# Kernel optimization log

Measured on AMD Instinct MI355X. Metric: run time of the kernel, lower is better.

The kernel has to match this reference:

```python
import jax, jax.numpy as jnp
import numpy as np

B = 16384
OBS = 568        # 36 self features + 19 * 28 other-agent features
H = 256          # hidden_dim
SELF_DIM = 36
OTHER_DIM = 28
N_OTHER = (OBS - SELF_DIM) // OTHER_DIM  # 19


def _linear_init(key, fan_in, fan_out):
    # torch nn.Linear default: U(-1/sqrt(fan_in), 1/sqrt(fan_in))
    kw, kb = jax.random.split(key)
    s = 1.0 / np.sqrt(fan_in)
    W = jax.random.uniform(kw, (fan_in, fan_out), jnp.float32, -s, s)
    b = jax.random.uniform(kb, (fan_out,), jnp.float32, -s, s)
    return W, b


def setup_inputs() -> dict:
    key = jax.random.key(0)
    ks = jax.random.split(key, 10)
    x = jax.random.normal(ks[0], (B, OBS), jnp.float32)
    eps = jax.random.normal(ks[1], (B, H), jnp.float32)
    W_mu, b_mu = _linear_init(ks[2], OBS, H)
    W_var, b_var = _linear_init(ks[3], OBS, H)
    W_self, b_self = _linear_init(ks[4], SELF_DIM, H)
    W_other, b_other = _linear_init(ks[5], OTHER_DIM, H)
    W_q, b_q = _linear_init(ks[6], H, H)
    W_k, b_k = _linear_init(ks[7], H, H)
    W_v, b_v = _linear_init(ks[8], 2 * H, H)
    W_a, b_a = _linear_init(ks[9], 2 * H, H)
    return {"x": x, "eps": eps,
            "W_mu": W_mu, "b_mu": b_mu, "W_var": W_var, "b_var": b_var,
            "W_self": W_self, "b_self": b_self, "W_other": W_other, "b_other": b_other,
            "W_q": W_q, "b_q": b_q, "W_k": W_k, "b_k": b_k,
            "W_v": W_v, "b_v": b_v, "W_a": W_a, "b_a": b_a}


def reference(x, eps, W_mu, b_mu, W_var, b_var, W_self, b_self,
              W_other, b_other, W_q, b_q, W_k, b_k, W_v, b_v, W_a, b_a):
    relu = jax.nn.relu
    # VAE reparameterization (detach=False path)
    mu = x @ W_mu + b_mu                                  # [B, H]
    log_var = x @ W_var + b_var                           # [B, H]
    z = eps * jnp.exp(0.5 * log_var) + mu                 # [B, H]

    self_info = x[:, :SELF_DIM]                           # [B, 36]
    agents_info = x[:, SELF_DIM:].reshape(B, N_OTHER, OTHER_DIM)  # [B, N, 28]

    self_em = relu(self_info @ W_self + b_self)           # [B, H]
    other_ems = relu(agents_info @ W_other + b_other)     # [B, N, H]

    q = relu(z @ W_q + b_q)                               # [B, H]
    k = relu(other_ems @ W_k + b_k)                       # [B, N, H]
    v_in = jnp.concatenate(
        [other_ems, jnp.broadcast_to(self_em[:, None, :], (B, N_OTHER, H))], axis=-1)
    v = relu(v_in @ W_v + b_v)                            # [B, N, H]

    scores = jnp.einsum('bh,bnh->bn', q, k) / np.sqrt(H)  # [B, N]
    att_weight = jax.nn.softmax(scores, axis=-1)          # [B, N]
    h = jnp.einsum('bn,bnh->bh', att_weight, v)           # [B, H]

    out = relu(jnp.concatenate([h, self_em], axis=-1) @ W_a + b_a)  # [B, H]
    return out, att_weight[:, None, :]                    # att: [B, 1, N]
```

## Files before the change

### kernel.cpp

```cpp
#include <hip/hip_runtime.h>

typedef __bf16 bf16;
typedef __bf16 bf16x4 __attribute__((ext_vector_type(4)));
typedef __bf16 bf16x8 __attribute__((ext_vector_type(8)));
typedef float  f32x4  __attribute__((ext_vector_type(4)));

#define NB    16384
#define NOBS  568
#define NH    256
#define NAG   19

#define OFF_WT_MU    0u
#define OFF_WT_VAR   294912u
#define OFF_WT_SELF  589824u
#define OFF_WT_OTHER 622592u
#define OFF_WT_Q     638976u
#define OFF_WT_K     770048u
#define OFF_WT_V1    901120u
#define OFF_WT_V2    1032192u
#define OFF_WT_A1    1163264u
#define OFF_WT_A2    1294336u
#define OFF_Z        1425408u
#define OFF_SELF     9814016u
#define OFF_Q        18202624u
#define OFF_SV       26591232u
#define OFF_H        34979840u

static __device__ __forceinline__ unsigned short bfbits(float v) {
  bf16 b = (bf16)v;
  union { bf16 b; unsigned short u; } cvt; cvt.b = b; return cvt.u;
}

static __device__ __forceinline__ void gload16(const bf16* g, bf16* l) {
  __builtin_amdgcn_global_load_lds(
      (const __attribute__((address_space(1))) void*)g,
      (__attribute__((address_space(3))) void*)(void*)l, 16, 0, 0);
}

__global__ __launch_bounds__(256) void wprep(
    const float* __restrict__ Wmu, const float* __restrict__ Wvar,
    const float* __restrict__ Wself, const float* __restrict__ Wother,
    const float* __restrict__ Wq, const float* __restrict__ Wk,
    const float* __restrict__ Wv, const float* __restrict__ Wa, char* wsb)
{
  const float* src; bf16* dst; int K, Kp; bool chunked = false;
  switch (blockIdx.y) {
    case 0: src = Wmu;        dst = (bf16*)(wsb + OFF_WT_MU);    K = 568; Kp = 576; break;
    case 1: src = Wvar;       dst = (bf16*)(wsb + OFF_WT_VAR);   K = 568; Kp = 576; break;
    case 2: src = Wself;      dst = (bf16*)(wsb + OFF_WT_SELF);  K = 36;  Kp = 64;  break;
    case 3: src = Wother;     dst = (bf16*)(wsb + OFF_WT_OTHER); K = 28;  Kp = 32;  break;
    case 4: src = Wq;         dst = (bf16*)(wsb + OFF_WT_Q);     K = 256; Kp = 256; chunked = true; break;
    case 5: src = Wk;         dst = (bf16*)(wsb + OFF_WT_K);     K = 256; Kp = 256; chunked = true; break;
    case 6: src = Wv;         dst = (bf16*)(wsb + OFF_WT_V1);    K = 256; Kp = 256; chunked = true; break;
    case 7: src = Wv + 65536; dst = (bf16*)(wsb + OFF_WT_V2);    K = 256; Kp = 256; chunked = true; break;
    case 8: src = Wa;         dst = (bf16*)(wsb + OFF_WT_A1);    K = 256; Kp = 256; chunked = true; break;
    default: src = Wa + 65536; dst = (bf16*)(wsb + OFF_WT_A2);   K = 256; Kp = 256; chunked = true; break;
  }
  int total = 256 * Kp;
  if (chunked) {
    for (int i = blockIdx.x * 256 + threadIdx.x; i < total; i += gridDim.x * 256) {
      int ch = i >> 13, n = (i >> 5) & 255, kk = i & 31;
      int k = ch * 32 + kk;
      dst[i] = (bf16)src[k * 256 + n];
    }
  } else {
    for (int i = blockIdx.x * 256 + threadIdx.x; i < total; i += gridDim.x * 256) {
      int n = i / Kp, k = i - n * Kp;
      dst[i] = (k < K) ? (bf16)src[k * 256 + n] : (bf16)0.f;
    }
  }
}

__global__ __launch_bounds__(256, 3) void gemm_zself(
    const float* __restrict__ x,
    const bf16* __restrict__ WtMu, const bf16* __restrict__ WtVar,
    const bf16* __restrict__ WtSelf,
    const float* __restrict__ b_mu, const float* __restrict__ b_var,
    const float* __restrict__ b_self, const float* __restrict__ eps,
    bf16* __restrict__ zout, bf16* __restrict__ selfout)
{
  __shared__ bf16 ldsA[64 * 40];
  __shared__ bf16 ldsB[128 * 40];
  __shared__ bf16 ldsB2[128 * 40];

  const int tid = threadIdx.x;
  const int wave = tid >> 6;
  const int lane = tid & 63;
  const int quad = lane >> 4;
  const int m = lane & 15;
  const int rowbase = blockIdx.x * 64;
  const int colbase = (blockIdx.y & 1) * 128;
  const bool isZ = blockIdx.y < 2;
  const int K = isZ ? 576 : 64;
  const bf16* __restrict__ Wt = isZ ? WtMu : WtSelf;
  const float* __restrict__ bias = isZ ? b_mu : b_self;

  f32x4 acc[8], accB[8];
  const f32x4 z4 = {0.f, 0.f, 0.f, 0.f};
#pragma unroll
  for (int ct = 0; ct < 8; ++ct) { acc[ct] = z4; accB[ct] = z4; }

  for (int kc = 0; kc < K; kc += 32) {
    __syncthreads();
    {
#pragma unroll
      for (int it = 0; it < 2; ++it) {
        int p = tid + 256 * it;
        int r = p >> 3, fs = p & 7;
        int k = kc + fs * 4;
        const float* src = x + (size_t)(rowbase + r) * 568 + k;
        float v0, v1, v2, v3;
        if (k + 4 <= 568) {
          float4 v = *(const float4*)src;
          v0 = v.x; v1 = v.y; v2 = v.z; v3 = v.w;
        } else {
          v0 = (k + 0 < 568) ? src[0] : 0.f;
          v1 = (k + 1 < 568) ? src[1] : 0.f;
          v2 = (k + 2 < 568) ? src[2] : 0.f;
          v3 = (k + 3 < 568) ? src[3] : 0.f;
        }
        bf16x4 o = {(bf16)v0, (bf16)v1, (bf16)v2, (bf16)v3};
        *(bf16x4*)(ldsA + r * 40 + fs * 4) = o;
      }
    }
#pragma unroll
    for (int it = 0; it < 2; ++it) {
      int p = tid + 256 * it;
      int n = p >> 2, f = p & 3;
      *(bf16x8*)(ldsB + n * 40 + f * 8) =
          *(const bf16x8*)(Wt + (size_t)(colbase + n) * K + kc + f * 8);
    }
    if (isZ) {
#pragma unroll
      for (int it = 0; it < 2; ++it) {
        int p = tid + 256 * it;
        int n = p >> 2, f = p & 3;
        *(bf16x8*)(ldsB2 + n * 40 + f * 8) =
            *(const bf16x8*)(WtVar + (size_t)(colbase + n) * 576 + kc + f * 8);
      }
    }
    __syncthreads();
    bf16x8 afrag = *(const bf16x8*)(ldsA + (wave * 16 + m) * 40 + quad * 8);
#pragma unroll
    for (int ct = 0; ct < 8; ++ct) {
      bf16x8 bfrag = *(const bf16x8*)(ldsB + (ct * 16 + m) * 40 + quad * 8);
      acc[ct] = __builtin_amdgcn_mfma_f32_16x16x32_bf16(afrag, bfrag, acc[ct], 0, 0, 0);
      if (isZ) {
        bf16x8 b2 = *(const bf16x8*)(ldsB2 + (ct * 16 + m) * 40 + quad * 8);
        accB[ct] = __builtin_amdgcn_mfma_f32_16x16x32_bf16(afrag, b2, accB[ct], 0, 0, 0);
      }
    }
  }
#pragma unroll
  for (int ct = 0; ct < 8; ++ct) {
    const int col = colbase + ct * 16 + m;
    const float bv = bias[col];
#pragma unroll
    for (int r = 0; r < 4; ++r) {
      const size_t row = (size_t)rowbase + wave * 16 + quad * 4 + r;
      float v = acc[ct][r] + bv;
      if (isZ) {
        float lv = accB[ct][r] + b_var[col];
        float zz = eps[row * 256 + col] * __expf(0.5f * lv) + v;
        zout[row * 256 + col] = (bf16)zz;
      } else {
        selfout[row * 256 + col] = (bf16)(v > 0.f ? v : 0.f);
      }
    }
  }
}

__global__ __launch_bounds__(256, 4) void gemm_qsv(
    const bf16* __restrict__ zb, const bf16* __restrict__ selfb,
    const bf16* __restrict__ WtQc, const bf16* __restrict__ WtV2c,
    const float* __restrict__ b_q, const float* __restrict__ b_v,
    bf16* __restrict__ qout, bf16* __restrict__ svout)
{
  __shared__ __align__(16) bf16 lA[2][64 * 32];
  __shared__ __align__(16) bf16 lB[2][128 * 32];

  const int tid = threadIdx.x;
  const int wave = tid >> 6;
  const int lane = tid & 63;
  const int quad = lane >> 4;
  const int m = lane & 15;
  const int rowbase = blockIdx.x * 64;
  const int colbase = (blockIdx.y & 1) * 128;
  const bool isQ = blockIdx.y < 2;
  const bf16* __restrict__ Ap = isQ ? zb : selfb;
  const bf16* __restrict__ Wc = isQ ? WtQc : WtV2c;
  const float* __restrict__ bias = isQ ? b_q : b_v;
  bf16* __restrict__ outp = isQ ? qout : svout;

  f32x4 acc[8];
  const f32x4 z4 = {0.f, 0.f, 0.f, 0.f};
#pragma unroll
  for (int ct = 0; ct < 8; ++ct) acc[ct] = z4;

  const size_t arow = (size_t)(rowbase + (tid >> 2)) * 256 + (tid & 3) * 8;
  const size_t bbase = (size_t)colbase * 32 + (size_t)tid * 8;

  gload16(Ap + arow, &lA[0][wave * 512]);
  gload16(Wc + bbase, &lB[0][wave * 512]);
  gload16(Wc + bbase + 2048, &lB[0][2048 + wave * 512]);
  __syncthreads();

#pragma unroll
  for (int ch = 0; ch < 8; ++ch) {
    const int cur = ch & 1;
    if (ch < 7) {
      const int nxt = cur ^ 1;
      const size_t cof = (size_t)(ch + 1) * 8192;
      gload16(Ap + arow + (ch + 1) * 32, &lA[nxt][wave * 512]);
      gload16(Wc + cof + bbase, &lB[nxt][wave * 512]);
      gload16(Wc + cof + bbase + 2048, &lB[nxt][2048 + wave * 512]);
    }
    bf16x8 afrag = *(const bf16x8*)(&lA[cur][(wave * 16 + m) * 32 + quad * 8]);
#pragma unroll
    for (int ct = 0; ct < 8; ++ct) {
      bf16x8 bfrag = *(const bf16x8*)(&lB[cur][(ct * 16 + m) * 32 + quad * 8]);
      acc[ct] = __builtin_amdgcn_mfma_f32_16x16x32_bf16(afrag, bfrag, acc[ct], 0, 0, 0);
    }
    __syncthreads();
  }

#pragma unroll
  for (int ct = 0; ct < 8; ++ct) {
    const int col = colbase + ct * 16 + m;
    const float bv = bias[col];
#pragma unroll
    for (int r = 0; r < 4; ++r) {
      const size_t row = (size_t)rowbase + wave * 16 + quad * 4 + r;
      float v = acc[ct][r] + bv;
      if (isQ) v = (v > 0.f ? v : 0.f);
      outp[row * 256 + col] = (bf16)v;
    }
  }
}

__global__ __launch_bounds__(256, 4) void gemm_dualA(
    const bf16* __restrict__ A1, const bf16* __restrict__ A2,
    const bf16* __restrict__ Wt1c, const bf16* __restrict__ Wt2c,
    const float* __restrict__ bias, float* __restrict__ outp)
{
  __shared__ __align__(16) bf16 lA[2][64 * 32];
  __shared__ __align__(16) bf16 lB[2][128 * 32];

  const int tid = threadIdx.x;
  const int wave = tid >> 6;
  const int lane = tid & 63;
  const int quad = lane >> 4;
  const int m = lane & 15;
  const int rowbase = blockIdx.x * 64;
  const int colbase = blockIdx.y * 128;

  f32x4 acc[8];
  const f32x4 z4 = {0.f, 0.f, 0.f, 0.f};
#pragma unroll
  for (int ct = 0; ct < 8; ++ct) acc[ct] = z4;

  const size_t arow = (size_t)(rowbase + (tid >> 2)) * 256 + (tid & 3) * 8;
  const size_t bbase = (size_t)colbase * 32 + (size_t)tid * 8;

  auto stageT = [&](int buf, int t) {
    const int ch = t & 7;
    const bf16* Astep = (t < 8) ? A1 : A2;
    const bf16* Wstep = (t < 8) ? Wt1c : Wt2c;
    const size_t cof = (size_t)ch * 8192;
    gload16(Astep + arow + ch * 32, &lA[buf][wave * 512]);
    gload16(Wstep + cof + bbase, &lB[buf][wave * 512]);
    gload16(Wstep + cof + bbase + 2048, &lB[buf][2048 + wave * 512]);
  };

  stageT(0, 0);
  __syncthreads();

#pragma unroll
  for (int t = 0; t < 16; ++t) {
    const int cur = t & 1;
    if (t < 15) stageT(cur ^ 1, t + 1);
    bf16x8 afrag = *(const bf16x8*)(&lA[cur][(wave * 16 + m) * 32 + quad * 8]);
#pragma unroll
    for (int ct = 0; ct < 8; ++ct) {
      bf16x8 bfrag = *(const bf16x8*)(&lB[cur][(ct * 16 + m) * 32 + quad * 8]);
      acc[ct] = __builtin_amdgcn_mfma_f32_16x16x32_bf16(afrag, bfrag, acc[ct], 0, 0, 0);
    }
    __syncthreads();
  }

#pragma unroll
  for (int ct = 0; ct < 8; ++ct) {
    const int col = colbase + ct * 16 + m;
    const float bv = bias[col];
#pragma unroll
    for (int r = 0; r < 4; ++r) {
      const size_t row = (size_t)rowbase + wave * 16 + quad * 4 + r;
      float v = acc[ct][r] + bv;
      outp[row * 256 + col] = (v > 0.f ? v : 0.f);
    }
  }
}

__global__ __launch_bounds__(512, 4) void k_fused(
    const float* __restrict__ x, const bf16* __restrict__ qb,
    const bf16* __restrict__ svb,
    const bf16* __restrict__ WtOther, const float* __restrict__ b_other,
    const bf16* __restrict__ WtKc, const float* __restrict__ b_k,
    const bf16* __restrict__ WtVc,
    float* __restrict__ att_out, bf16* __restrict__ hb)
{
  __shared__ bf16 ldsO[80 * 264];
  __shared__ bf16 ldsA1[80 * 40];
  __shared__ bf16 qh16[1024];
  __shared__ bf16 svl16[1024];
  float* spart = (float*)ldsA1;
  float* attl  = (float*)ldsA1 + 320;

  const int tid = threadIdx.x, wave = tid >> 6, lane = tid & 63;
  const int quad = lane >> 4, m = lane & 15;
  const int b0 = blockIdx.x * 4;
  const int kvw = wave & 3;
  const bool isV = wave >= 4;

  ((unsigned*)qh16)[tid]  = ((const unsigned*)(qb  + (size_t)b0 * 256))[tid];
  ((unsigned*)svl16)[tid] = ((const unsigned*)(svb + (size_t)b0 * 256))[tid];
  for (int i = tid; i < 80 * 16; i += 512) {
    int r = i >> 4, kk = (i & 15) * 2;
    int n = r >> 2, bb = r & 3;
    float v0 = 0.f, v1 = 0.f;
    if (n < 19) {
      const float* base = x + (size_t)(b0 + bb) * NOBS + 36 + n * 28;
      if (kk < 28) v0 = base[kk];
      if (kk + 1 < 28) v1 = base[kk + 1];
    }
    unsigned u0 = bfbits(v0), u1 = bfbits(v1);
    *(unsigned*)(ldsA1 + r * 40 + kk) = u0 | (u1 << 16);
  }

  const f32x4 z4 = {0.f, 0.f, 0.f, 0.f};

  const bf16* __restrict__ Bc = isV ? WtVc : WtKc;
  const int cb = (kvw * 64 + m) * 32 + quad * 8;
  bf16x8 bE[4];
#pragma unroll
  for (int c = 0; c < 4; ++c) bE[c] = *(const bf16x8*)(Bc + cb + c * 512);

  __syncthreads();

  {
    float bo[2];
    bf16x8 bfr[2];
#pragma unroll
    for (int c = 0; c < 2; ++c) {
      int col = (2 * wave + c) * 16 + m;
      bo[c] = b_other[col];
      bfr[c] = *(const bf16x8*)(WtOther + col * 32 + quad * 8);
    }
    f32x4 acc1[5][2];
#pragma unroll
    for (int rt = 0; rt < 5; ++rt) {
      bf16x8 a = *(const bf16x8*)(ldsA1 + (rt * 16 + m) * 40 + quad * 8);
#pragma unroll
      for (int c = 0; c < 2; ++c)
        acc1[rt][c] = __builtin_amdgcn_mfma_f32_16x16x32_bf16(a, bfr[c], z4, 0, 0, 0);
    }
#pragma unroll
    for (int rt = 0; rt < 5; ++rt)
#pragma unroll
      for (int c = 0; c < 2; ++c) {
        int col = (2 * wave + c) * 16 + m;
#pragma unroll
        for (int r = 0; r < 4; ++r) {
          float v = acc1[rt][c][r] + bo[c];
          v = v > 0.f ? v : 0.f;
          unsigned u = bfbits(v);
          unsigned other = (unsigned)__shfl_xor((int)u, 1, 64);
          if ((m & 1) == 0) {
            int rowl = rt * 16 + quad * 4 + r;
            *(unsigned*)(ldsO + rowl * 264 + col) = u | (other << 16);
          }
        }
      }
  }
  __syncthreads();

  f32x4 acc[5][4];
#pragma unroll
  for (int rt = 0; rt < 5; ++rt)
#pragma unroll
    for (int c = 0; c < 4; ++c) acc[rt][c] = z4;

  {
#pragma unroll 1
    for (int ch = 0; ch < 8; ch += 2) {
      bf16x8 bO[4];
#pragma unroll
      for (int c = 0; c < 4; ++c)
        bO[c] = *(const bf16x8*)(Bc + (size_t)(ch + 1) * 8192 + cb + c * 512);
      const int kc0 = ch * 32;
#pragma unroll
      for (int rt = 0; rt < 5; ++rt) {
        bf16x8 a = *(const bf16x8*)(ldsO + (rt * 16 + m) * 264 + kc0 + quad * 8);
#pragma unroll
        for (int c = 0; c < 4; ++c)
          acc[rt][c] = __builtin_amdgcn_mfma_f32_16x16x32_bf16(a, bE[c], acc[rt][c], 0, 0, 0);
      }
#pragma unroll
      for (int c = 0; c < 4; ++c)
        bE[c] = *(const bf16x8*)(Bc + (size_t)(ch + 2) * 8192 + cb + c * 512);
      const int kc1 = kc0 + 32;
#pragma unroll
      for (int rt = 0; rt < 5; ++rt) {
        bf16x8 a = *(const bf16x8*)(ldsO + (rt * 16 + m) * 264 + kc1 + quad * 8);
#pragma unroll
        for (int c = 0; c < 4; ++c)
          acc[rt][c] = __builtin_amdgcn_mfma_f32_16x16x32_bf16(a, bO[c], acc[rt][c], 0, 0, 0);
      }
    }
  }

  if (!isV) {
    float qreg[4][4], bkreg[4];
#pragma unroll
    for (int c = 0; c < 4; ++c) {
      int col = (4 * wave + c) * 16 + m;
      bkreg[c] = b_k[col];
#pragma unroll
      for (int r = 0; r < 4; ++r) qreg[c][r] = (float)qh16[r * 256 + col];
    }
#pragma unroll
    for (int rt = 0; rt < 5; ++rt) {
      float part[4] = {0.f, 0.f, 0.f, 0.f};
#pragma unroll
      for (int c = 0; c < 4; ++c) {
#pragma unroll
        for (int r = 0; r < 4; ++r) {
          float kv = acc[rt][c][r] + bkreg[c];
          kv = kv > 0.f ? kv : 0.f;
          part[r] += kv * qreg[c][r];
        }
      }
#pragma unroll
      for (int r = 0; r < 4; ++r) {
        float p = part[r];
        p += __shfl_xor(p, 1, 64);
        p += __shfl_xor(p, 2, 64);
        p += __shfl_xor(p, 4, 64);
        p += __shfl_xor(p, 8, 64);
        if (m == 0) spart[wave * 80 + rt * 16 + quad * 4 + r] = p;
      }
    }
  }
  __syncthreads();

  if (!isV && lane < 32) {
    const int bb = wave, j = lane;
    float s = -1e30f;
    if (j < 19) {
      int row = j * 4 + bb;
      s = (spart[row] + spart[80 + row] + spart[160 + row] + spart[240 + row]) * 0.0625f;
    }
    float mx = s;
#pragma unroll
    for (int off = 16; off >= 1; off >>= 1) mx = fmaxf(mx, __shfl_xor(mx, off, 32));
    float e = (j < 19) ? __expf(s - mx) : 0.f;
    float sum = e;
#pragma unroll
    for (int off = 16; off >= 1; off >>= 1) sum += __shfl_xor(sum, off, 32);
    float inv = 1.f / sum;
    float a = e * inv;
    if (j < 20) attl[j * 4 + bb] = a;
    if (j < 19) att_out[(size_t)(b0 + bb) * 19 + j] = a;
  }
  __syncthreads();

  if (isV) {
    float svreg[4][4];
#pragma unroll
    for (int c = 0; c < 4; ++c) {
      int col = (4 * kvw + c) * 16 + m;
#pragma unroll
      for (int r = 0; r < 4; ++r) svreg[c][r] = (float)svl16[r * 256 + col];
    }
    float hacc[4][4];
#pragma unroll
    for (int c = 0; c < 4; ++c)
#pragma unroll
      for (int r = 0; r < 4; ++r) hacc[c][r] = 0.f;
#pragma unroll
    for (int rt = 0; rt < 5; ++rt) {
      float av[4];
#pragma unroll
      for (int r = 0; r < 4; ++r) av[r] = attl[rt * 16 + quad * 4 + r];
#pragma unroll
      for (int c = 0; c < 4; ++c) {
#pragma unroll
        for (int r = 0; r < 4; ++r) {
          float v = acc[rt][c][r] + svreg[c][r];
          v = v > 0.f ? v : 0.f;
          hacc[c][r] += v * av[r];
        }
      }
    }
#pragma unroll
    for (int c = 0; c < 4; ++c)
#pragma unroll
      for (int r = 0; r < 4; ++r) {
        float h = hacc[c][r];
        h += __shfl_xor(h, 16, 64);
        h += __shfl_xor(h, 32, 64);
        if (quad == 0) qh16[r * 256 + (4 * kvw + c) * 16 + m] = (bf16)h;
      }
  }
  __syncthreads();
  ((unsigned*)(hb + (size_t)b0 * 256))[tid] = ((const unsigned*)qh16)[tid];
}

extern "C" void kernel_launch(void* const* d_in, const int* in_sizes, int n_in,
                              void* d_out, int out_size, void* d_ws, size_t ws_size,
                              hipStream_t stream) {
  (void)in_sizes; (void)n_in; (void)out_size; (void)ws_size;
  const float* x      = (const float*)d_in[0];
  const float* eps    = (const float*)d_in[1];
  const float* W_mu   = (const float*)d_in[2];
  const float* b_mu   = (const float*)d_in[3];
  const float* W_var  = (const float*)d_in[4];
  const float* b_var  = (const float*)d_in[5];
  const float* W_self = (const float*)d_in[6];
  const float* b_self = (const float*)d_in[7];
  const float* W_other= (const float*)d_in[8];
  const float* b_other= (const float*)d_in[9];
  const float* W_q    = (const float*)d_in[10];
  const float* b_q    = (const float*)d_in[11];
  const float* W_k    = (const float*)d_in[12];
  const float* b_k    = (const float*)d_in[13];
  const float* W_v    = (const float*)d_in[14];
  const float* b_v    = (const float*)d_in[15];
  const float* W_a    = (const float*)d_in[16];
  const float* b_a    = (const float*)d_in[17];

  char* wsb = (char*)d_ws;
  bf16* WtMu    = (bf16*)(wsb + OFF_WT_MU);
  bf16* WtVar   = (bf16*)(wsb + OFF_WT_VAR);
  bf16* WtSelf  = (bf16*)(wsb + OFF_WT_SELF);
  bf16* WtOther = (bf16*)(wsb + OFF_WT_OTHER);
  bf16* WtQ     = (bf16*)(wsb + OFF_WT_Q);
  bf16* WtK     = (bf16*)(wsb + OFF_WT_K);
  bf16* WtV1    = (bf16*)(wsb + OFF_WT_V1);
  bf16* WtV2    = (bf16*)(wsb + OFF_WT_V2);
  bf16* WtA1    = (bf16*)(wsb + OFF_WT_A1);
  bf16* WtA2    = (bf16*)(wsb + OFF_WT_A2);
  bf16* zbuf    = (bf16*)(wsb + OFF_Z);
  bf16* selfbuf = (bf16*)(wsb + OFF_SELF);
  bf16* qbuf    = (bf16*)(wsb + OFF_Q);
  bf16* svbuf   = (bf16*)(wsb + OFF_SV);
  bf16* hbuf    = (bf16*)(wsb + OFF_H);

  float* out = (float*)d_out;
  float* att_out = out + (size_t)NB * 256;

  dim3 blk(256);
  wprep<<<dim3(160, 10), blk, 0, stream>>>(W_mu, W_var, W_self, W_other, W_q, W_k, W_v, W_a, wsb);
  gemm_zself<<<dim3(NB / 64, 4), blk, 0, stream>>>(x, WtMu, WtVar, WtSelf,
                                                   b_mu, b_var, b_self, eps, zbuf, selfbuf);
  gemm_qsv<<<dim3(NB / 64, 4), blk, 0, stream>>>(zbuf, selfbuf, WtQ, WtV2,
                                                 b_q, b_v, qbuf, svbuf);
  k_fused<<<NB / 4, dim3(512), 0, stream>>>(x, qbuf, svbuf, WtOther, b_other, WtK, b_k,
                                            WtV1, att_out, hbuf);
  gemm_dualA<<<dim3(NB / 64, 2), blk, 0, stream>>>(hbuf, selfbuf, WtA1, WtA2, b_a, out);
}
```

Measured before the change: 336.6 us.

## Fuse q/self-value GEMM and output projection into attention kernel

Removes the separate gemm_qsv and gemm_dualA launches and computes q, the self part of v, and the final W_a projection inside k_fused for each 4-row batch tile. This drops the q/sv/h intermediate buffers and their global round trips, and cuts two kernel launches. In exchange each block runs 16-row MFMAs with only 4 valid rows, which wastes matrix throughput, and it streams the full W_q/W_v2/W_a weights from global or L2 per block with no LDS reuse across row tiles.

```diff
diff --git a/kernel.cpp b/kernel.cpp
--- a/kernel.cpp
+++ b/kernel.cpp
@@ -29,12 +29,6 @@
 static __device__ __forceinline__ unsigned short bfbits(float v) {
   bf16 b = (bf16)v;
   union { bf16 b; unsigned short u; } cvt; cvt.b = b; return cvt.u;
-}
-
-static __device__ __forceinline__ void gload16(const bf16* g, bf16* l) {
-  __builtin_amdgcn_global_load_lds(
-      (const __attribute__((address_space(1))) void*)g,
-      (__attribute__((address_space(3))) void*)(void*)l, 16, 0, 0);
 }
 
 __global__ __launch_bounds__(256) void wprep(
@@ -170,144 +164,17 @@
   }
 }
 
-__global__ __launch_bounds__(256, 4) void gemm_qsv(
+__global__ __launch_bounds__(512, 4) void k_fused(
+    const float* __restrict__ x,
     const bf16* __restrict__ zb, const bf16* __restrict__ selfb,
-    const bf16* __restrict__ WtQc, const bf16* __restrict__ WtV2c,
-    const float* __restrict__ b_q, const float* __restrict__ b_v,
-    bf16* __restrict__ qout, bf16* __restrict__ svout)
-{
-  __shared__ __align__(16) bf16 lA[2][64 * 32];
-  __shared__ __align__(16) bf16 lB[2][128 * 32];
-
-  const int tid = threadIdx.x;
-  const int wave = tid >> 6;
-  const int lane = tid & 63;
-  const int quad = lane >> 4;
-  const int m = lane & 15;
-  const int rowbase = blockIdx.x * 64;
-  const int colbase = (blockIdx.y & 1) * 128;
-  const bool isQ = blockIdx.y < 2;
-  const bf16* __restrict__ Ap = isQ ? zb : selfb;
-  const bf16* __restrict__ Wc = isQ ? WtQc : WtV2c;
-  const float* __restrict__ bias = isQ ? b_q : b_v;
-  bf16* __restrict__ outp = isQ ? qout : svout;
-
-  f32x4 acc[8];
-  const f32x4 z4 = {0.f, 0.f, 0.f, 0.f};
-#pragma unroll
-  for (int ct = 0; ct < 8; ++ct) acc[ct] = z4;
-
-  const size_t arow = (size_t)(rowbase + (tid >> 2)) * 256 + (tid & 3) * 8;
-  const size_t bbase = (size_t)colbase * 32 + (size_t)tid * 8;
-
-  gload16(Ap + arow, &lA[0][wave * 512]);
-  gload16(Wc + bbase, &lB[0][wave * 512]);
-  gload16(Wc + bbase + 2048, &lB[0][2048 + wave * 512]);
-  __syncthreads();
-
-#pragma unroll
-  for (int ch = 0; ch < 8; ++ch) {
-    const int cur = ch & 1;
-    if (ch < 7) {
-      const int nxt = cur ^ 1;
-      const size_t cof = (size_t)(ch + 1) * 8192;
-      gload16(Ap + arow + (ch + 1) * 32, &lA[nxt][wave * 512]);
-      gload16(Wc + cof + bbase, &lB[nxt][wave * 512]);
-      gload16(Wc + cof + bbase + 2048, &lB[nxt][2048 + wave * 512]);
-    }
-    bf16x8 afrag = *(const bf16x8*)(&lA[cur][(wave * 16 + m) * 32 + quad * 8]);
-#pragma unroll
-    for (int ct = 0; ct < 8; ++ct) {
-      bf16x8 bfrag = *(const bf16x8*)(&lB[cur][(ct * 16 + m) * 32 + quad * 8]);
-      acc[ct] = __builtin_amdgcn_mfma_f32_16x16x32_bf16(afrag, bfrag, acc[ct], 0, 0, 0);
-    }
-    __syncthreads();
-  }
-
-#pragma unroll
-  for (int ct = 0; ct < 8; ++ct) {
-    const int col = colbase + ct * 16 + m;
-    const float bv = bias[col];
-#pragma unroll
-    for (int r = 0; r < 4; ++r) {
-      const size_t row = (size_t)rowbase + wave * 16 + quad * 4 + r;
-      float v = acc[ct][r] + bv;
-      if (isQ) v = (v > 0.f ? v : 0.f);
-      outp[row * 256 + col] = (bf16)v;
-    }
-  }
-}
-
-__global__ __launch_bounds__(256, 4) void gemm_dualA(
-    const bf16* __restrict__ A1, const bf16* __restrict__ A2,
-    const bf16* __restrict__ Wt1c, const bf16* __restrict__ Wt2c,
-    const float* __restrict__ bias, float* __restrict__ outp)
-{
-  __shared__ __align__(16) bf16 lA[2][64 * 32];
-  __shared__ __align__(16) bf16 lB[2][128 * 32];
-
-  const int tid = threadIdx.x;
-  const int wave = tid >> 6;
-  const int lane = tid & 63;
-  const int quad = lane >> 4;
-  const int m = lane & 15;
-  const int rowbase = blockIdx.x * 64;
-  const int colbase = blockIdx.y * 128;
-
-  f32x4 acc[8];
-  const f32x4 z4 = {0.f, 0.f, 0.f, 0.f};
-#pragma unroll
-  for (int ct = 0; ct < 8; ++ct) acc[ct] = z4;
-
-  const size_t arow = (size_t)(rowbase + (tid >> 2)) * 256 + (tid & 3) * 8;
-  const size_t bbase = (size_t)colbase * 32 + (size_t)tid * 8;
-
-  auto stageT = [&](int buf, int t) {
-    const int ch = t & 7;
-    const bf16* Astep = (t < 8) ? A1 : A2;
-    const bf16* Wstep = (t < 8) ? Wt1c : Wt2c;
-    const size_t cof = (size_t)ch * 8192;
-    gload16(Astep + arow + ch * 32, &lA[buf][wave * 512]);
-    gload16(Wstep + cof + bbase, &lB[buf][wave * 512]);
-    gload16(Wstep + cof + bbase + 2048, &lB[buf][2048 + wave * 512]);
-  };
-
-  stageT(0, 0);
-  __syncthreads();
-
-#pragma unroll
-  for (int t = 0; t < 16; ++t) {
-    const int cur = t & 1;
-    if (t < 15) stageT(cur ^ 1, t + 1);
-    bf16x8 afrag = *(const bf16x8*)(&lA[cur][(wave * 16 + m) * 32 + quad * 8]);
-#pragma unroll
-    for (int ct = 0; ct < 8; ++ct) {
-      bf16x8 bfrag = *(const bf16x8*)(&lB[cur][(ct * 16 + m) * 32 + quad * 8]);
-      acc[ct] = __builtin_amdgcn_mfma_f32_16x16x32_bf16(afrag, bfrag, acc[ct], 0, 0, 0);
-    }
-    __syncthreads();
-  }
-
-#pragma unroll
-  for (int ct = 0; ct < 8; ++ct) {
-    const int col = colbase + ct * 16 + m;
-    const float bv = bias[col];
-#pragma unroll
-    for (int r = 0; r < 4; ++r) {
-      const size_t row = (size_t)rowbase + wave * 16 + quad * 4 + r;
-      float v = acc[ct][r] + bv;
-      outp[row * 256 + col] = (v > 0.f ? v : 0.f);
-    }
-  }
-}
-
-__global__ __launch_bounds__(512, 4) void k_fused(
-    const float* __restrict__ x, const bf16* __restrict__ qb,
-    const bf16* __restrict__ svb,
     const bf16* __restrict__ WtOther, const float* __restrict__ b_other,
     const bf16* __restrict__ WtKc, const float* __restrict__ b_k,
     const bf16* __restrict__ WtVc,
-    float* __restrict__ att_out, bf16* __restrict__ hb)
+    const bf16* __restrict__ WtQc, const float* __restrict__ b_q,
+    const bf16* __restrict__ WtV2c, const float* __restrict__ b_v,
+    const bf16* __restrict__ WtA1c, const bf16* __restrict__ WtA2c,
+    const float* __restrict__ b_a,
+    float* __restrict__ att_out, float* __restrict__ outp)
 {
   __shared__ bf16 ldsO[80 * 264];
   __shared__ bf16 ldsA1[80 * 40];
@@ -322,8 +189,6 @@
   const int kvw = wave & 3;
   const bool isV = wave >= 4;
 
-  ((unsigned*)qh16)[tid]  = ((const unsigned*)(qb  + (size_t)b0 * 256))[tid];
-  ((unsigned*)svl16)[tid] = ((const unsigned*)(svb + (size_t)b0 * 256))[tid];
   for (int i = tid; i < 80 * 16; i += 512) {
     int r = i >> 4, kk = (i & 15) * 2;
     int n = r >> 2, bb = r & 3;
@@ -344,6 +209,12 @@
   bf16x8 bE[4];
 #pragma unroll
   for (int c = 0; c < 4; ++c) bE[c] = *(const bf16x8*)(Bc + cb + c * 512);
+
+  const bf16* __restrict__ Wm = isV ? WtV2c : WtQc;
+  const bf16* __restrict__ Am = isV ? selfb : zb;
+  bf16x8 mE[4];
+#pragma unroll
+  for (int c = 0; c < 4; ++c) mE[c] = *(const bf16x8*)(Wm + cb + c * 512);
 
   __syncthreads();
 
@@ -382,6 +253,47 @@
         }
       }
   }
+
+  {
+    f32x4 macc[4];
+#pragma unroll
+    for (int c = 0; c < 4; ++c) macc[c] = z4;
+    const bf16* arow = Am + (size_t)(b0 + (m & 3)) * 256 + quad * 8;
+#pragma unroll 1
+    for (int ch = 0; ch < 8; ch += 2) {
+      bf16x8 mO[4];
+#pragma unroll
+      for (int c = 0; c < 4; ++c)
+        mO[c] = *(const bf16x8*)(Wm + (size_t)(ch + 1) * 8192 + cb + c * 512);
+      bf16x8 ma0 = *(const bf16x8*)(arow + ch * 32);
+#pragma unroll
+      for (int c = 0; c < 4; ++c)
+        macc[c] = __builtin_amdgcn_mfma_f32_16x16x32_bf16(ma0, mE[c], macc[c], 0, 0, 0);
+#pragma unroll
+      for (int c = 0; c < 4; ++c)
+        mE[c] = *(const bf16x8*)(Wm + (size_t)(ch + 2) * 8192 + cb + c * 512);
+      bf16x8 ma1 = *(const bf16x8*)(arow + (ch + 1) * 32);
+#pragma unroll
+      for (int c = 0; c < 4; ++c)
+        macc[c] = __builtin_amdgcn_mfma_f32_16x16x32_bf16(ma1, mO[c], macc[c], 0, 0, 0);
+    }
+    const float* bm = isV ? b_v : b_q;
+    bf16* dst = isV ? svl16 : qh16;
+#pragma unroll
+    for (int c = 0; c < 4; ++c) {
+      int col = kvw * 64 + c * 16 + m;
+      float bv = bm[col];
+#pragma unroll
+      for (int r = 0; r < 4; ++r) {
+        float v = macc[c][r] + bv;
+        if (!isV) v = v > 0.f ? v : 0.f;
+        unsigned u = bfbits(v);
+        unsigned other = (unsigned)__shfl_xor((int)u, 1, 64);
+        if (quad == 0 && (m & 1) == 0)
+          *(unsigned*)(dst + r * 256 + col) = u | (other << 16);
+      }
+    }
+  }
   __syncthreads();
 
   f32x4 acc[5][4];
@@ -418,6 +330,11 @@
       }
     }
   }
+
+  const int ocb = (wave * 32 + m) * 32 + quad * 8;
+  bf16x8 oE[2];
+#pragma unroll
+  for (int c = 0; c < 2; ++c) oE[c] = *(const bf16x8*)(WtA1c + ocb + c * 512);
 
   if (!isV) {
     float qreg[4][4], bkreg[4];
@@ -513,7 +430,50 @@
       }
   }
   __syncthreads();
-  ((unsigned*)(hb + (size_t)b0 * 256))[tid] = ((const unsigned*)qh16)[tid];
+
+  {
+    f32x4 oacc[2];
+#pragma unroll
+    for (int c = 0; c < 2; ++c) oacc[c] = z4;
+    const bf16* srow = selfb + (size_t)(b0 + (m & 3)) * 256 + quad * 8;
+#pragma unroll 1
+    for (int t = 0; t < 16; t += 2) {
+      bf16x8 oO[2];
+      const bf16* Wn1 = (t + 1 < 8) ? WtA1c : WtA2c;
+#pragma unroll
+      for (int c = 0; c < 2; ++c)
+        oO[c] = *(const bf16x8*)(Wn1 + (size_t)((t + 1) & 7) * 8192 + ocb + c * 512);
+      bf16x8 oa0, oa1;
+      if (t < 8) {
+        oa0 = *(const bf16x8*)(qh16 + (m & 3) * 256 + t * 32 + quad * 8);
+        oa1 = *(const bf16x8*)(qh16 + (m & 3) * 256 + (t + 1) * 32 + quad * 8);
+      } else {
+        oa0 = *(const bf16x8*)(srow + (t - 8) * 32);
+        oa1 = *(const bf16x8*)(srow + (t - 7) * 32);
+      }
+#pragma unroll
+      for (int c = 0; c < 2; ++c)
+        oacc[c] = __builtin_amdgcn_mfma_f32_16x16x32_bf16(oa0, oE[c], oacc[c], 0, 0, 0);
+      const bf16* Wn2 = (t + 2 < 8) ? WtA1c : WtA2c;
+#pragma unroll
+      for (int c = 0; c < 2; ++c)
+        oE[c] = *(const bf16x8*)(Wn2 + (size_t)((t + 2) & 7) * 8192 + ocb + c * 512);
+#pragma unroll
+      for (int c = 0; c < 2; ++c)
+        oacc[c] = __builtin_amdgcn_mfma_f32_16x16x32_bf16(oa1, oO[c], oacc[c], 0, 0, 0);
+    }
+#pragma unroll
+    for (int c = 0; c < 2; ++c) {
+      const int col = wave * 32 + c * 16 + m;
+      const float bv = b_a[col];
+#pragma unroll
+      for (int r = 0; r < 4; ++r) {
+        float v = oacc[c][r] + bv;
+        v = v > 0.f ? v : 0.f;
+        if (quad == 0) outp[(size_t)(b0 + r) * 256 + col] = v;
+      }
+    }
+  }
 }
 
 extern "C" void kernel_launch(void* const* d_in, const int* in_sizes, int n_in,
@@ -552,9 +512,6 @@
   bf16* WtA2    = (bf16*)(wsb + OFF_WT_A2);
   bf16* zbuf    = (bf16*)(wsb + OFF_Z);
   bf16* selfbuf = (bf16*)(wsb + OFF_SELF);
-  bf16* qbuf    = (bf16*)(wsb + OFF_Q);
-  bf16* svbuf   = (bf16*)(wsb + OFF_SV);
-  bf16* hbuf    = (bf16*)(wsb + OFF_H);
 
   float* out = (float*)d_out;
   float* att_out = out + (size_t)NB * 256;
@@ -563,9 +520,8 @@
   wprep<<<dim3(160, 10), blk, 0, stream>>>(W_mu, W_var, W_self, W_other, W_q, W_k, W_v, W_a, wsb);
   gemm_zself<<<dim3(NB / 64, 4), blk, 0, stream>>>(x, WtMu, WtVar, WtSelf,
                                                    b_mu, b_var, b_self, eps, zbuf, selfbuf);
-  gemm_qsv<<<dim3(NB / 64, 4), blk, 0, stream>>>(zbuf, selfbuf, WtQ, WtV2,
-                                                 b_q, b_v, qbuf, svbuf);
-  k_fused<<<NB / 4, dim3(512), 0, stream>>>(x, qbuf, svbuf, WtOther, b_other, WtK, b_k,
-                                            WtV1, att_out, hbuf);
-  gemm_dualA<<<dim3(NB / 64, 2), blk, 0, stream>>>(hbuf, selfbuf, WtA1, WtA2, b_a, out);
+  k_fused<<<NB / 4, dim3(512), 0, stream>>>(x, zbuf, selfbuf,
+                                            WtOther, b_other, WtK, b_k, WtV1,
+                                            WtQ, b_q, WtV2, b_v, WtA1, WtA2, b_a,
+                                            att_out, out);
 }
```

After: 482.1 us. +43.3%, slower.

## Fuse z/self GEMM with q/sv GEMM, keeping intermediate tile in LDS

Applied to the files above, without the earlier changes.

Merges the z/self projection kernel and the q/sv projection kernel into one kernel. Each block now computes all 256 output columns for its 64 rows, stages the bf16 z (or self) tile in LDS, and immediately runs the second GEMM against W_q or W_v2, with the weights read straight from global memory into registers. This removes one kernel launch and the global write and re-read of the z buffer. The cost is a halved grid, twice the accumulator registers (launch bounds drop to 2 blocks per CU), and the x tile no longer being shared across column blocks, which may hurt occupancy.

```diff
diff --git a/kernel.cpp b/kernel.cpp
--- a/kernel.cpp
+++ b/kernel.cpp
@@ -71,17 +71,22 @@
   }
 }
 
-__global__ __launch_bounds__(256, 3) void gemm_zself(
+__global__ __launch_bounds__(256, 2) void gemm_zq(
     const float* __restrict__ x,
     const bf16* __restrict__ WtMu, const bf16* __restrict__ WtVar,
     const bf16* __restrict__ WtSelf,
+    const bf16* __restrict__ WtQc, const bf16* __restrict__ WtV2c,
     const float* __restrict__ b_mu, const float* __restrict__ b_var,
-    const float* __restrict__ b_self, const float* __restrict__ eps,
-    bf16* __restrict__ zout, bf16* __restrict__ selfout)
+    const float* __restrict__ b_self,
+    const float* __restrict__ b_q, const float* __restrict__ b_v,
+    const float* __restrict__ eps,
+    bf16* __restrict__ qout, bf16* __restrict__ selfout, bf16* __restrict__ svout)
 {
   __shared__ bf16 ldsA[64 * 40];
-  __shared__ bf16 ldsB[128 * 40];
-  __shared__ bf16 ldsB2[128 * 40];
+  __shared__ bf16 ldsBU[2 * 256 * 40];
+  bf16* ldsB  = ldsBU;
+  bf16* ldsB2 = ldsBU + 256 * 40;
+  bf16* zl    = ldsBU;
 
   const int tid = threadIdx.x;
   const int wave = tid >> 6;
@@ -89,18 +94,16 @@
   const int quad = lane >> 4;
   const int m = lane & 15;
   const int rowbase = blockIdx.x * 64;
-  const int colbase = (blockIdx.y & 1) * 128;
-  const bool isZ = blockIdx.y < 2;
-  const int K = isZ ? 576 : 64;
-  const bf16* __restrict__ Wt = isZ ? WtMu : WtSelf;
-  const float* __restrict__ bias = isZ ? b_mu : b_self;
-
-  f32x4 acc[8], accB[8];
+  const bool isZ = blockIdx.y == 0;
+  const int KA = isZ ? 576 : 64;
+  const bf16* __restrict__ W1 = isZ ? WtMu : WtSelf;
+
   const f32x4 z4 = {0.f, 0.f, 0.f, 0.f};
-#pragma unroll
-  for (int ct = 0; ct < 8; ++ct) { acc[ct] = z4; accB[ct] = z4; }
-
-  for (int kc = 0; kc < K; kc += 32) {
+  f32x4 a1[16], a2[16];
+#pragma unroll
+  for (int ct = 0; ct < 16; ++ct) { a1[ct] = z4; a2[ct] = z4; }
+
+  for (int kc = 0; kc < KA; kc += 32) {
     __syncthreads();
     {
 #pragma unroll
@@ -124,117 +127,118 @@
       }
     }
 #pragma unroll
-    for (int it = 0; it < 2; ++it) {
+    for (int it = 0; it < 4; ++it) {
       int p = tid + 256 * it;
       int n = p >> 2, f = p & 3;
       *(bf16x8*)(ldsB + n * 40 + f * 8) =
-          *(const bf16x8*)(Wt + (size_t)(colbase + n) * K + kc + f * 8);
+          *(const bf16x8*)(W1 + (size_t)n * KA + kc + f * 8);
     }
     if (isZ) {
 #pragma unroll
-      for (int it = 0; it < 2; ++it) {
+      for (int it = 0; it < 4; ++it) {
         int p = tid + 256 * it;
         int n = p >> 2, f = p & 3;
         *(bf16x8*)(ldsB2 + n * 40 + f * 8) =
-            *(const bf16x8*)(WtVar + (size_t)(colbase + n) * 576 + kc + f * 8);
+            *(const bf16x8*)(WtVar + (size_t)n * 576 + kc + f * 8);
       }
     }
     __syncthreads();
     bf16x8 afrag = *(const bf16x8*)(ldsA + (wave * 16 + m) * 40 + quad * 8);
 #pragma unroll
-    for (int ct = 0; ct < 8; ++ct) {
+    for (int ct = 0; ct < 16; ++ct) {
       bf16x8 bfrag = *(const bf16x8*)(ldsB + (ct * 16 + m) * 40 + quad * 8);
-      acc[ct] = __builtin_amdgcn_mfma_f32_16x16x32_bf16(afrag, bfrag, acc[ct], 0, 0, 0);
+      a1[ct] = __builtin_amdgcn_mfma_f32_16x16x32_bf16(afrag, bfrag, a1[ct], 0, 0, 0);
       if (isZ) {
         bf16x8 b2 = *(const bf16x8*)(ldsB2 + (ct * 16 + m) * 40 + quad * 8);
-        accB[ct] = __builtin_amdgcn_mfma_f32_16x16x32_bf16(afrag, b2, accB[ct], 0, 0, 0);
-      }
-    }
-  }
-#pragma unroll
-  for (int ct = 0; ct < 8; ++ct) {
-    const int col = colbase + ct * 16 + m;
-    const float bv = bias[col];
+        a2[ct] = __builtin_amdgcn_mfma_f32_16x16x32_bf16(afrag, b2, a2[ct], 0, 0, 0);
+      }
+    }
+  }
+  __syncthreads();
+
+#pragma unroll
+  for (int ct = 0; ct < 16; ++ct) {
+    const int col = ct * 16 + m;
+    const float bv1 = isZ ? b_mu[col] : b_self[col];
+    const float bv2 = isZ ? b_var[col] : 0.f;
 #pragma unroll
     for (int r = 0; r < 4; ++r) {
-      const size_t row = (size_t)rowbase + wave * 16 + quad * 4 + r;
-      float v = acc[ct][r] + bv;
+      const int rowl = wave * 16 + quad * 4 + r;
+      const size_t row = (size_t)rowbase + rowl;
+      float v;
       if (isZ) {
-        float lv = accB[ct][r] + b_var[col];
-        float zz = eps[row * 256 + col] * __expf(0.5f * lv) + v;
-        zout[row * 256 + col] = (bf16)zz;
+        float mu = a1[ct][r] + bv1;
+        float lv = a2[ct][r] + bv2;
+        v = eps[row * 256 + col] * __expf(0.5f * lv) + mu;
       } else {
-        selfout[row * 256 + col] = (bf16)(v > 0.f ? v : 0.f);
-      }
-    }
-  }
-}
-
-__global__ __launch_bounds__(256, 4) void gemm_qsv(
-    const bf16* __restrict__ zb, const bf16* __restrict__ selfb,
-    const bf16* __restrict__ WtQc, const bf16* __restrict__ WtV2c,
-    const float* __restrict__ b_q, const float* __restrict__ b_v,
-    bf16* __restrict__ qout, bf16* __restrict__ svout)
-{
-  __shared__ __align__(16) bf16 lA[2][64 * 32];
-  __shared__ __align__(16) bf16 lB[2][128 * 32];
-
-  const int tid = threadIdx.x;
-  const int wave = tid >> 6;
-  const int lane = tid & 63;
-  const int quad = lane >> 4;
-  const int m = lane & 15;
-  const int rowbase = blockIdx.x * 64;
-  const int colbase = (blockIdx.y & 1) * 128;
-  const bool isQ = blockIdx.y < 2;
-  const bf16* __restrict__ Ap = isQ ? zb : selfb;
-  const bf16* __restrict__ Wc = isQ ? WtQc : WtV2c;
-  const float* __restrict__ bias = isQ ? b_q : b_v;
-  bf16* __restrict__ outp = isQ ? qout : svout;
-
-  f32x4 acc[8];
-  const f32x4 z4 = {0.f, 0.f, 0.f, 0.f};
-#pragma unroll
-  for (int ct = 0; ct < 8; ++ct) acc[ct] = z4;
-
-  const size_t arow = (size_t)(rowbase + (tid >> 2)) * 256 + (tid & 3) * 8;
-  const size_t bbase = (size_t)colbase * 32 + (size_t)tid * 8;
-
-  gload16(Ap + arow, &lA[0][wave * 512]);
-  gload16(Wc + bbase, &lB[0][wave * 512]);
-  gload16(Wc + bbase + 2048, &lB[0][2048 + wave * 512]);
-  __syncthreads();
-
-#pragma unroll
-  for (int ch = 0; ch < 8; ++ch) {
-    const int cur = ch & 1;
-    if (ch < 7) {
-      const int nxt = cur ^ 1;
-      const size_t cof = (size_t)(ch + 1) * 8192;
-      gload16(Ap + arow + (ch + 1) * 32, &lA[nxt][wave * 512]);
-      gload16(Wc + cof + bbase, &lB[nxt][wave * 512]);
-      gload16(Wc + cof + bbase + 2048, &lB[nxt][2048 + wave * 512]);
-    }
-    bf16x8 afrag = *(const bf16x8*)(&lA[cur][(wave * 16 + m) * 32 + quad * 8]);
-#pragma unroll
-    for (int ct = 0; ct < 8; ++ct) {
-      bf16x8 bfrag = *(const bf16x8*)(&lB[cur][(ct * 16 + m) * 32 + quad * 8]);
-      acc[ct] = __builtin_amdgcn_mfma_f32_16x16x32_bf16(afrag, bfrag, acc[ct], 0, 0, 0);
-    }
-    __syncthreads();
-  }
-
-#pragma unroll
-  for (int ct = 0; ct < 8; ++ct) {
-    const int col = colbase + ct * 16 + m;
-    const float bv = bias[col];
-#pragma unroll
-    for (int r = 0; r < 4; ++r) {
-      const size_t row = (size_t)rowbase + wave * 16 + quad * 4 + r;
-      float v = acc[ct][r] + bv;
-      if (isQ) v = (v > 0.f ? v : 0.f);
-      outp[row * 256 + col] = (bf16)v;
-    }
+        v = a1[ct][r] + bv1;
+        v = v > 0.f ? v : 0.f;
+      }
+      unsigned u = bfbits(v);
+      unsigned other = (unsigned)__shfl_xor((int)u, 1, 64);
+      if ((m & 1) == 0) {
+        unsigned pk = u | (other << 16);
+        *(unsigned*)(zl + rowl * 264 + col) = pk;
+        if (!isZ) *(unsigned*)(selfout + row * 256 + col) = pk;
+      }
+    }
+  }
+  __syncthreads();
+
+  {
+    const bf16* __restrict__ W3 = isZ ? WtQc : WtV2c;
+    const int cb = (wave * 64 + m) * 32 + quad * 8;
+    f32x4 oacc[4][4];
+#pragma unroll
+    for (int rt = 0; rt < 4; ++rt)
+#pragma unroll
+      for (int c = 0; c < 4; ++c) oacc[rt][c] = z4;
+    bf16x8 pE[4];
+#pragma unroll
+    for (int c = 0; c < 4; ++c) pE[c] = *(const bf16x8*)(W3 + cb + c * 512);
+#pragma unroll 1
+    for (int ch = 0; ch < 8; ch += 2) {
+      bf16x8 pO[4];
+#pragma unroll
+      for (int c = 0; c < 4; ++c)
+        pO[c] = *(const bf16x8*)(W3 + (size_t)(ch + 1) * 8192 + cb + c * 512);
+#pragma unroll
+      for (int rt = 0; rt < 4; ++rt) {
+        bf16x8 a = *(const bf16x8*)(zl + (rt * 16 + m) * 264 + ch * 32 + quad * 8);
+#pragma unroll
+        for (int c = 0; c < 4; ++c)
+          oacc[rt][c] = __builtin_amdgcn_mfma_f32_16x16x32_bf16(a, pE[c], oacc[rt][c], 0, 0, 0);
+      }
+#pragma unroll
+      for (int c = 0; c < 4; ++c)
+        pE[c] = *(const bf16x8*)(W3 + (size_t)(ch + 2) * 8192 + cb + c * 512);
+#pragma unroll
+      for (int rt = 0; rt < 4; ++rt) {
+        bf16x8 a = *(const bf16x8*)(zl + (rt * 16 + m) * 264 + (ch + 1) * 32 + quad * 8);
+#pragma unroll
+        for (int c = 0; c < 4; ++c)
+          oacc[rt][c] = __builtin_amdgcn_mfma_f32_16x16x32_bf16(a, pO[c], oacc[rt][c], 0, 0, 0);
+      }
+    }
+    const float* __restrict__ b3 = isZ ? b_q : b_v;
+    bf16* __restrict__ out3 = isZ ? qout : svout;
+#pragma unroll
+    for (int rt = 0; rt < 4; ++rt)
+#pragma unroll
+      for (int c = 0; c < 4; ++c) {
+        const int col = wave * 64 + c * 16 + m;
+        const float bv = b3[col];
+#pragma unroll
+        for (int r = 0; r < 4; ++r) {
+          const size_t row = (size_t)rowbase + rt * 16 + quad * 4 + r;
+          float v = oacc[rt][c][r] + bv;
+          if (isZ) v = v > 0.f ? v : 0.f;
+          unsigned u = bfbits(v);
+          unsigned other = (unsigned)__shfl_xor((int)u, 1, 64);
+          if ((m & 1) == 0)
+            *(unsigned*)(out3 + row * 256 + col) = u | (other << 16);
+        }
+      }
   }
 }
 
@@ -550,7 +554,6 @@
   bf16* WtV2    = (bf16*)(wsb + OFF_WT_V2);
   bf16* WtA1    = (bf16*)(wsb + OFF_WT_A1);
   bf16* WtA2    = (bf16*)(wsb + OFF_WT_A2);
-  bf16* zbuf    = (bf16*)(wsb + OFF_Z);
   bf16* selfbuf = (bf16*)(wsb + OFF_SELF);
   bf16* qbuf    = (bf16*)(wsb + OFF_Q);
   bf16* svbuf   = (bf16*)(wsb + OFF_SV);
@@ -561,10 +564,9 @@
 
   dim3 blk(256);
   wprep<<<dim3(160, 10), blk, 0, stream>>>(W_mu, W_var, W_self, W_other, W_q, W_k, W_v, W_a, wsb);
-  gemm_zself<<<dim3(NB / 64, 4), blk, 0, stream>>>(x, WtMu, WtVar, WtSelf,
-                                                   b_mu, b_var, b_self, eps, zbuf, selfbuf);
-  gemm_qsv<<<dim3(NB / 64, 4), blk, 0, stream>>>(zbuf, selfbuf, WtQ, WtV2,
-                                                 b_q, b_v, qbuf, svbuf);
+  gemm_zq<<<dim3(NB / 64, 2), blk, 0, stream>>>(x, WtMu, WtVar, WtSelf, WtQ, WtV2,
+                                                b_mu, b_var, b_self, b_q, b_v, eps,
+                                                qbuf, selfbuf, svbuf);
   k_fused<<<NB / 4, dim3(512), 0, stream>>>(x, qbuf, svbuf, WtOther, b_other, WtK, b_k,
                                             WtV1, att_out, hbuf);
   gemm_dualA<<<dim3(NB / 64, 2), blk, 0, stream>>>(hbuf, selfbuf, WtA1, WtA2, b_a, out);
```

Result: slower. 354.6 us (+5.4%).

## Double-buffer gemm_zself and stage chunked weights via direct global-to-LDS loads

Applied to the files above, without the earlier changes.

Weight prep now stores every weight in a K-chunked layout (32-wide chunks, n-major within a chunk), so each chunk's B tile is contiguous. gemm_zself double-buffers the A and B tiles in LDS. It issues global_load_lds for the next chunk's weights and register prefetch of the next x tile before computing the current chunk, leaving one barrier per iteration. The aim is to hide global load latency behind MFMA work. The cost is more LDS use and an unpadded 32-wide B stride, which may cause bank conflicts. Other kernels that read the mu/var/self/other weights must accept the new layout.

```diff
diff --git a/kernel.cpp b/kernel.cpp
--- a/kernel.cpp
+++ b/kernel.cpp
@@ -43,45 +43,38 @@
     const float* __restrict__ Wq, const float* __restrict__ Wk,
     const float* __restrict__ Wv, const float* __restrict__ Wa, char* wsb)
 {
-  const float* src; bf16* dst; int K, Kp; bool chunked = false;
+  const float* src; bf16* dst; int K, Kp;
   switch (blockIdx.y) {
     case 0: src = Wmu;        dst = (bf16*)(wsb + OFF_WT_MU);    K = 568; Kp = 576; break;
     case 1: src = Wvar;       dst = (bf16*)(wsb + OFF_WT_VAR);   K = 568; Kp = 576; break;
     case 2: src = Wself;      dst = (bf16*)(wsb + OFF_WT_SELF);  K = 36;  Kp = 64;  break;
     case 3: src = Wother;     dst = (bf16*)(wsb + OFF_WT_OTHER); K = 28;  Kp = 32;  break;
-    case 4: src = Wq;         dst = (bf16*)(wsb + OFF_WT_Q);     K = 256; Kp = 256; chunked = true; break;
-    case 5: src = Wk;         dst = (bf16*)(wsb + OFF_WT_K);     K = 256; Kp = 256; chunked = true; break;
-    case 6: src = Wv;         dst = (bf16*)(wsb + OFF_WT_V1);    K = 256; Kp = 256; chunked = true; break;
-    case 7: src = Wv + 65536; dst = (bf16*)(wsb + OFF_WT_V2);    K = 256; Kp = 256; chunked = true; break;
-    case 8: src = Wa;         dst = (bf16*)(wsb + OFF_WT_A1);    K = 256; Kp = 256; chunked = true; break;
-    default: src = Wa + 65536; dst = (bf16*)(wsb + OFF_WT_A2);   K = 256; Kp = 256; chunked = true; break;
+    case 4: src = Wq;         dst = (bf16*)(wsb + OFF_WT_Q);     K = 256; Kp = 256; break;
+    case 5: src = Wk;         dst = (bf16*)(wsb + OFF_WT_K);     K = 256; Kp = 256; break;
+    case 6: src = Wv;         dst = (bf16*)(wsb + OFF_WT_V1);    K = 256; Kp = 256; break;
+    case 7: src = Wv + 65536; dst = (bf16*)(wsb + OFF_WT_V2);    K = 256; Kp = 256; break;
+    case 8: src = Wa;         dst = (bf16*)(wsb + OFF_WT_A1);    K = 256; Kp = 256; break;
+    default: src = Wa + 65536; dst = (bf16*)(wsb + OFF_WT_A2);   K = 256; Kp = 256; break;
   }
   int total = 256 * Kp;
-  if (chunked) {
-    for (int i = blockIdx.x * 256 + threadIdx.x; i < total; i += gridDim.x * 256) {
-      int ch = i >> 13, n = (i >> 5) & 255, kk = i & 31;
-      int k = ch * 32 + kk;
-      dst[i] = (bf16)src[k * 256 + n];
-    }
-  } else {
-    for (int i = blockIdx.x * 256 + threadIdx.x; i < total; i += gridDim.x * 256) {
-      int n = i / Kp, k = i - n * Kp;
-      dst[i] = (k < K) ? (bf16)src[k * 256 + n] : (bf16)0.f;
-    }
+  for (int i = blockIdx.x * 256 + threadIdx.x; i < total; i += gridDim.x * 256) {
+    int n = i & 255, kk = (i >> 8) & 31, ch = i >> 13;
+    int k = ch * 32 + kk;
+    dst[ch * 8192 + n * 32 + kk] = (k < K) ? (bf16)src[k * 256 + n] : (bf16)0.f;
   }
 }
 
 __global__ __launch_bounds__(256, 3) void gemm_zself(
     const float* __restrict__ x,
-    const bf16* __restrict__ WtMu, const bf16* __restrict__ WtVar,
-    const bf16* __restrict__ WtSelf,
+    const bf16* __restrict__ WtMuC, const bf16* __restrict__ WtVarC,
+    const bf16* __restrict__ WtSelfC,
     const float* __restrict__ b_mu, const float* __restrict__ b_var,
     const float* __restrict__ b_self, const float* __restrict__ eps,
     bf16* __restrict__ zout, bf16* __restrict__ selfout)
 {
-  __shared__ bf16 ldsA[64 * 40];
-  __shared__ bf16 ldsB[128 * 40];
-  __shared__ bf16 ldsB2[128 * 40];
+  __shared__ bf16 lA[2][64 * 40];
+  __shared__ __align__(16) bf16 lB1[2][128 * 32];
+  __shared__ __align__(16) bf16 lB2[2][128 * 32];
 
   const int tid = threadIdx.x;
   const int wave = tid >> 6;
@@ -91,8 +84,8 @@
   const int rowbase = blockIdx.x * 64;
   const int colbase = (blockIdx.y & 1) * 128;
   const bool isZ = blockIdx.y < 2;
-  const int K = isZ ? 576 : 64;
-  const bf16* __restrict__ Wt = isZ ? WtMu : WtSelf;
+  const int nch = isZ ? 18 : 2;
+  const bf16* __restrict__ W1 = isZ ? WtMuC : WtSelfC;
   const float* __restrict__ bias = isZ ? b_mu : b_self;
 
   f32x4 acc[8], accB[8];
@@ -100,57 +93,72 @@
 #pragma unroll
   for (int ct = 0; ct < 8; ++ct) { acc[ct] = z4; accB[ct] = z4; }
 
-  for (int kc = 0; kc < K; kc += 32) {
-    __syncthreads();
-    {
-#pragma unroll
-      for (int it = 0; it < 2; ++it) {
-        int p = tid + 256 * it;
-        int r = p >> 3, fs = p & 7;
-        int k = kc + fs * 4;
-        const float* src = x + (size_t)(rowbase + r) * 568 + k;
-        float v0, v1, v2, v3;
-        if (k + 4 <= 568) {
-          float4 v = *(const float4*)src;
-          v0 = v.x; v1 = v.y; v2 = v.z; v3 = v.w;
-        } else {
-          v0 = (k + 0 < 568) ? src[0] : 0.f;
-          v1 = (k + 1 < 568) ? src[1] : 0.f;
-          v2 = (k + 2 < 568) ? src[2] : 0.f;
-          v3 = (k + 3 < 568) ? src[3] : 0.f;
-        }
-        bf16x4 o = {(bf16)v0, (bf16)v1, (bf16)v2, (bf16)v3};
-        *(bf16x4*)(ldsA + r * 40 + fs * 4) = o;
-      }
-    }
-#pragma unroll
-    for (int it = 0; it < 2; ++it) {
-      int p = tid + 256 * it;
-      int n = p >> 2, f = p & 3;
-      *(bf16x8*)(ldsB + n * 40 + f * 8) =
-          *(const bf16x8*)(Wt + (size_t)(colbase + n) * K + kc + f * 8);
-    }
+  const int ar0 = tid >> 3, afs0 = tid & 7;
+  const int ar1 = (tid + 256) >> 3, afs1 = (tid + 256) & 7;
+
+  auto loadA = [&](int kc, int fs, int r, float4& f) {
+    int k = kc + fs * 4;
+    const float* src = x + (size_t)(rowbase + r) * 568 + k;
+    if (k + 4 <= 568) {
+      f = *(const float4*)src;
+    } else {
+      f.x = (k + 0 < 568) ? src[0] : 0.f;
+      f.y = (k + 1 < 568) ? src[1] : 0.f;
+      f.z = (k + 2 < 568) ? src[2] : 0.f;
+      f.w = (k + 3 < 568) ? src[3] : 0.f;
+    }
+  };
+  auto writeA = [&](int buf, int fs, int r, const float4& f) {
+    bf16x4 o = {(bf16)f.x, (bf16)f.y, (bf16)f.z, (bf16)f.w};
+    *(bf16x4*)(&lA[buf][r * 40 + fs * 4]) = o;
+  };
+  auto stageB = [&](int buf, int ch) {
+    const bf16* s1 = W1 + (size_t)ch * 8192 + colbase * 32 + tid * 8;
+    gload16(s1, &lB1[buf][wave * 512]);
+    gload16(s1 + 2048, &lB1[buf][2048 + wave * 512]);
     if (isZ) {
-#pragma unroll
-      for (int it = 0; it < 2; ++it) {
-        int p = tid + 256 * it;
-        int n = p >> 2, f = p & 3;
-        *(bf16x8*)(ldsB2 + n * 40 + f * 8) =
-            *(const bf16x8*)(WtVar + (size_t)(colbase + n) * 576 + kc + f * 8);
-      }
-    }
-    __syncthreads();
-    bf16x8 afrag = *(const bf16x8*)(ldsA + (wave * 16 + m) * 40 + quad * 8);
+      const bf16* s2 = WtVarC + (size_t)ch * 8192 + colbase * 32 + tid * 8;
+      gload16(s2, &lB2[buf][wave * 512]);
+      gload16(s2 + 2048, &lB2[buf][2048 + wave * 512]);
+    }
+  };
+
+  {
+    float4 f0, f1;
+    loadA(0, afs0, ar0, f0);
+    loadA(0, afs1, ar1, f1);
+    stageB(0, 0);
+    writeA(0, afs0, ar0, f0);
+    writeA(0, afs1, ar1, f1);
+  }
+  __syncthreads();
+
+  for (int ch = 0; ch < nch; ++ch) {
+    const int cur = ch & 1, nxt = cur ^ 1;
+    float4 f0, f1;
+    const bool more = (ch + 1 < nch);
+    if (more) {
+      stageB(nxt, ch + 1);
+      loadA((ch + 1) * 32, afs0, ar0, f0);
+      loadA((ch + 1) * 32, afs1, ar1, f1);
+    }
+    bf16x8 afrag = *(const bf16x8*)(&lA[cur][(wave * 16 + m) * 40 + quad * 8]);
 #pragma unroll
     for (int ct = 0; ct < 8; ++ct) {
-      bf16x8 bfrag = *(const bf16x8*)(ldsB + (ct * 16 + m) * 40 + quad * 8);
+      bf16x8 bfrag = *(const bf16x8*)(&lB1[cur][(ct * 16 + m) * 32 + quad * 8]);
       acc[ct] = __builtin_amdgcn_mfma_f32_16x16x32_bf16(afrag, bfrag, acc[ct], 0, 0, 0);
       if (isZ) {
-        bf16x8 b2 = *(const bf16x8*)(ldsB2 + (ct * 16 + m) * 40 + quad * 8);
+        bf16x8 b2 = *(const bf16x8*)(&lB2[cur][(ct * 16 + m) * 32 + quad * 8]);
         accB[ct] = __builtin_amdgcn_mfma_f32_16x16x32_bf16(afrag, b2, accB[ct], 0, 0, 0);
       }
     }
-  }
+    if (more) {
+      writeA(nxt, afs0, ar0, f0);
+      writeA(nxt, afs1, ar1, f1);
+    }
+    __syncthreads();
+  }
+
 #pragma unroll
   for (int ct = 0; ct < 8; ++ct) {
     const int col = colbase + ct * 16 + m;
```

Result: faster. 328.0 us (-2.5%).
